# Kernel optimization log

Measured on AMD Instinct MI355X. Metric: run time of the kernel, lower is better.

Reference implementation:

```python
import jax, jax.numpy as jnp
import numpy as np

D_MODEL = 128
N_HEADS = 4
HEAD_DIM = D_MODEL // N_HEADS


def setup_inputs() -> dict:
    key = jax.random.key(0)
    ks = jax.random.split(key, 16)
    s = 0.05
    B, N, T = 1, 1024, 1024
    return {
        "node_states": jax.random.normal(ks[0], (B, N, D_MODEL), jnp.float32),
        "task_features": jax.random.normal(ks[1], (T, D_MODEL), jnp.float32),
        "in_proj_w": jax.random.normal(ks[2], (3 * D_MODEL, D_MODEL), jnp.float32) * s,
        "in_proj_b": jnp.zeros((3 * D_MODEL,), jnp.float32),
        "out_w": jax.random.normal(ks[3], (D_MODEL, D_MODEL), jnp.float32) * s,
        "out_b": jnp.zeros((D_MODEL,), jnp.float32),
        "W1": jax.random.normal(ks[4], (256, 256), jnp.float32) * s,
        "b1": jnp.zeros((256,), jnp.float32),
        "W2": jax.random.normal(ks[5], (128, 256), jnp.float32) * s,
        "b2": jnp.zeros((128,), jnp.float32),
        "W3": jax.random.normal(ks[6], (1, 128), jnp.float32) * s,
        "b3": jnp.zeros((1,), jnp.float32),
        "Wc1": jax.random.normal(ks[7], (256, D_MODEL), jnp.float32) * s,
        "bc1": jnp.zeros((256,), jnp.float32),
        "Wc2": jax.random.normal(ks[8], (32, 256), jnp.float32) * s,
        "bc2": jnp.zeros((32,), jnp.float32),
    }


def _mha(x, in_proj_w, in_proj_b, out_w, out_b):
    # x: [B, N, D]; torch nn.MultiheadAttention self-attention, batch_first.
    B, N, D = x.shape
    q = x @ in_proj_w[:D].T + in_proj_b[:D]
    k = x @ in_proj_w[D:2 * D].T + in_proj_b[D:2 * D]
    v = x @ in_proj_w[2 * D:].T + in_proj_b[2 * D:]
    def split(t):  # [B,N,D] -> [B,H,N,dh]
        return t.reshape(B, N, N_HEADS, HEAD_DIM).transpose(0, 2, 1, 3)
    qh, kh, vh = split(q), split(k), split(v)
    scores = jnp.einsum("bhqd,bhkd->bhqk", qh, kh) / jnp.sqrt(jnp.float32(HEAD_DIM))
    attn = jax.nn.softmax(scores, axis=-1)  # [B,H,N,N]
    ctx = jnp.einsum("bhqk,bhkd->bhqd", attn, vh)
    ctx = ctx.transpose(0, 2, 1, 3).reshape(B, N, D)
    out = ctx @ out_w.T + out_b
    attn_avg = attn.mean(axis=1)  # torch averages heads by default -> [B,N,N]
    return out, attn_avg


def reference(node_states, task_features, in_proj_w, in_proj_b, out_w, out_b,
              W1, b1, W2, b2, W3, b3, Wc1, bc1, Wc2, bc2):
    attended, attn_w = _mha(node_states, in_proj_w, in_proj_b, out_w, out_b)
    nodes = attended[0]  # original loop only uses batch 0: [N, D]
    # Linear on concat([task, node]) == split-weight sum; vectorize pairwise.
    t1 = task_features @ W1[:, :D_MODEL].T          # [T, 256]
    n1 = nodes @ W1[:, D_MODEL:].T                  # [N, 256]
    h1 = jax.nn.relu(t1[:, None, :] + n1[None, :, :] + b1)      # [T, N, 256]
    h2 = jax.nn.relu(jnp.einsum("tnc,kc->tnk", h1, W2) + b2)   # [T, N, 128]
    matching_scores = jax.nn.sigmoid(jnp.einsum("tnk,ok->tn", h2, W3) + b3[0])
    global_state = attended.mean(axis=1)            # [B, D]
    coordination_logits = jax.nn.relu(global_state @ Wc1.T + bc1) @ Wc2.T + bc2
    return matching_scores, coordination_logits, attn_w
```

## Files before the change

### kernel.cpp

```cpp
#include <hip/hip_runtime.h>
#include <hip/hip_fp16.h>
#include <stdint.h>


typedef __attribute__((ext_vector_type(4))) float floatx4;
typedef __attribute__((ext_vector_type(8))) _Float16 half8;

#define OFF_QKV  0x000000u
#define OFF_Q16  0x180000u
#define OFF_K16  0x1C0000u
#define OFF_V16  0x200000u
#define OFF_T1H  0x280000u
#define OFF_N1H  0x300000u
#define OFF_W2F  0x380000u
#define OFF_GS   0x398000u
#define OFF_SC   0x400000u
#define OFF_CTP  0xC00000u

__device__ __forceinline__ unsigned pkadd(unsigned a, unsigned b) {
    unsigned r; asm("v_pk_add_f16 %0, %1, %2" : "=v"(r) : "v"(a), "v"(b)); return r;
}
__device__ __forceinline__ unsigned pkmax(unsigned a, unsigned b) {
    unsigned r; asm("v_pk_max_f16 %0, %1, %2" : "=v"(r) : "v"(a), "v"(b)); return r;
}
__device__ __forceinline__ unsigned pk2h(float a, float b) {
    return (unsigned)__half_as_ushort(__float2half(a)) |
           ((unsigned)__half_as_ushort(__float2half(b)) << 16);
}
__device__ __forceinline__ float h2f(unsigned short u) {
    return __half2float(__ushort_as_half(u));
}
__device__ __forceinline__ unsigned short f2h(float v) {
    return __half_as_ushort(__float2half(v));
}

template<bool BIAS, bool F16OUT, bool SIDE>
__device__ __forceinline__ void gemm_dev(
    const float* __restrict__ A, int lda,
    const float* __restrict__ B, int ldb,
    const float* __restrict__ bias,
    void* __restrict__ Cv, int ldc, int K, float scale,
    int m0, int n0, float (*As)[64], float (*Bs)[64],
    unsigned short* __restrict__ q16o,
    unsigned short* __restrict__ k16o,
    unsigned short* __restrict__ v16o)
{
    const int tid = threadIdx.x;
    const int tx = tid & 15, ty = tid >> 4;
    const int lr = tid >> 2;
    const int lk = (tid & 3) * 4;
    float c[4][4] = {};

    for (int k0 = 0; k0 < K; k0 += 16) {
        float4 a  = *(const float4*)&A[(long)(m0 + lr) * lda + k0 + lk];
        float4 bb = *(const float4*)&B[(long)(n0 + lr) * ldb + k0 + lk];
        __syncthreads();
        As[lk + 0][lr] = a.x;  As[lk + 1][lr] = a.y;  As[lk + 2][lr] = a.z;  As[lk + 3][lr] = a.w;
        Bs[lk + 0][lr] = bb.x; Bs[lk + 1][lr] = bb.y; Bs[lk + 2][lr] = bb.z; Bs[lk + 3][lr] = bb.w;
        __syncthreads();
#pragma unroll
        for (int k = 0; k < 16; k++) {
            float4 av = *(const float4*)&As[k][ty * 4];
            float4 bv = *(const float4*)&Bs[k][tx * 4];
            c[0][0] += av.x * bv.x; c[0][1] += av.x * bv.y; c[0][2] += av.x * bv.z; c[0][3] += av.x * bv.w;
            c[1][0] += av.y * bv.x; c[1][1] += av.y * bv.y; c[1][2] += av.y * bv.z; c[1][3] += av.y * bv.w;
            c[2][0] += av.z * bv.x; c[2][1] += av.z * bv.y; c[2][2] += av.z * bv.z; c[2][3] += av.z * bv.w;
            c[3][0] += av.w * bv.x; c[3][1] += av.w * bv.y; c[3][2] += av.w * bv.z; c[3][3] += av.w * bv.w;
        }
    }

    float bsv[4] = {0.f, 0.f, 0.f, 0.f};
    if (BIAS) {
        float4 t = *(const float4*)&bias[n0 + tx * 4];
        bsv[0] = t.x; bsv[1] = t.y; bsv[2] = t.z; bsv[3] = t.w;
    }
    const int gcol = n0 + tx * 4;
#pragma unroll
    for (int i = 0; i < 4; i++) {
        float v0 = c[i][0] * scale + bsv[0];
        float v1 = c[i][1] * scale + bsv[1];
        float v2 = c[i][2] * scale + bsv[2];
        float v3 = c[i][3] * scale + bsv[3];
        long m = m0 + ty * 4 + i;
        if (F16OUT) {
            unsigned short* Cp = (unsigned short*)Cv;
            ushort4 o;
            o.x = f2h(v0); o.y = f2h(v1); o.z = f2h(v2); o.w = f2h(v3);
            *(ushort4*)&Cp[m * ldc + n0 + tx * 4] = o;
        } else {
            float* Cp = (float*)Cv;
            *(float4*)&Cp[m * ldc + n0 + tx * 4] = make_float4(v0, v1, v2, v3);
        }
        if (SIDE) {
            ushort4 o;
            o.x = f2h(v0); o.y = f2h(v1); o.z = f2h(v2); o.w = f2h(v3);
            if (gcol < 128) {
                *(ushort4*)&q16o[m * 128 + gcol] = o;
            } else if (gcol < 256) {
                *(ushort4*)&k16o[m * 128 + (gcol - 128)] = o;
            } else {
                v16o[(size_t)(gcol - 256 + 0) * 1024 + m] = o.x;
                v16o[(size_t)(gcol - 256 + 1) * 1024 + m] = o.y;
                v16o[(size_t)(gcol - 256 + 2) * 1024 + m] = o.z;
                v16o[(size_t)(gcol - 256 + 3) * 1024 + m] = o.w;
            }
        }
    }
}

__launch_bounds__(256)
__global__ void proj_fused(const float* __restrict__ node, const float* __restrict__ ipw,
                           const float* __restrict__ ipb,
                           const float* __restrict__ task, const float* __restrict__ W1,
                           const float* __restrict__ b1, const float* __restrict__ W2,
                           float* __restrict__ qkv, unsigned short* __restrict__ t1h,
                           unsigned short* __restrict__ w2f, float* __restrict__ gs,
                           unsigned short* __restrict__ q16,
                           unsigned short* __restrict__ k16,
                           unsigned short* __restrict__ v16t)
{
    __shared__ float As[16][64], Bs[16][64];
    const int bid = blockIdx.x;
    if (bid < 96) {
        gemm_dev<true, false, true>(node, 128, ipw, 128, ipb, qkv, 384, 128, 1.0f,
                                    (bid & 15) * 64, (bid >> 4) * 64, As, Bs,
                                    q16, k16, v16t);
    } else if (bid < 160) {
        const int b = bid - 96;
        gemm_dev<true, true, false>(task, 128, W1, 256, b1, t1h, 256, 128, 1.0f,
                                    (b & 15) * 64, (b >> 4) * 64, As, Bs,
                                    nullptr, nullptr, nullptr);
    } else if (bid < 176) {
        const int gtid = (bid - 160) * 256 + threadIdx.x;
        const int lane = gtid & 63, frag = gtid >> 6;
        const int cc = frag >> 3, ot = frag & 7;
        const float* src = &W2[(ot * 16 + (lane & 15)) * 256 + cc * 32 + (lane >> 4) * 8];
        uint4 o;
        o.x = pk2h(src[0], src[1]);
        o.y = pk2h(src[2], src[3]);
        o.z = pk2h(src[4], src[5]);
        o.w = pk2h(src[6], src[7]);
        ((uint4*)w2f)[gtid] = o;
    } else {
        if (threadIdx.x < 128) gs[threadIdx.x] = 0.f;
    }
}

__launch_bounds__(256)
__global__ void scores_mfma(const unsigned short* __restrict__ q16,
                            const unsigned short* __restrict__ k16,
                            unsigned short* __restrict__ sc16)
{
    const int h = blockIdx.z;
    const int tid = threadIdx.x;
    const int lane = tid & 63, wv = tid >> 6;
    const int col = lane & 15, quad = lane >> 4;
    const int q0 = blockIdx.x * 64 + wv * 16;
    const int kb = blockIdx.y * 64;
    unsigned short* dst = sc16 + ((size_t)h << 20);

    union { uint4 u; half8 h8; } bf;
    bf.u = *(const uint4*)&q16[(size_t)(q0 + col) * 128 + h * 32 + quad * 8];
#pragma unroll
    for (int kt = 0; kt < 4; kt++) {
        union { uint4 u; half8 h8; } af;
        af.u = *(const uint4*)&k16[(size_t)(kb + kt * 16 + col) * 128 + h * 32 + quad * 8];
        floatx4 c = {0.f, 0.f, 0.f, 0.f};
        c = __builtin_amdgcn_mfma_f32_16x16x32_f16(af.h8, bf.h8, c, 0, 0, 0);
        ushort4 o;
        o.x = f2h(c[0] * 0.17677669529663687f);
        o.y = f2h(c[1] * 0.17677669529663687f);
        o.z = f2h(c[2] * 0.17677669529663687f);
        o.w = f2h(c[3] * 0.17677669529663687f);
        *(ushort4*)&dst[(size_t)(q0 + col) * 1024 + kb + kt * 16 + quad * 4] = o;
    }
}

__launch_bounds__(256)
__global__ void attn_pre(const unsigned short* __restrict__ sc16,
                         unsigned short* __restrict__ pb,
                         float* __restrict__ attn_out)
{
    __shared__ float Ps[4][1024];
    __shared__ float stm[4], stl[4];
    const int t = threadIdx.x;
    const int q = blockIdx.x;

#pragma unroll
    for (int h = 0; h < 4; h++) {
        ushort4 u = *(const ushort4*)&sc16[((size_t)h << 20) + (size_t)q * 1024 + t * 4];
        *(float4*)&Ps[h][t * 4] = make_float4(h2f(u.x), h2f(u.y), h2f(u.z), h2f(u.w));
    }
    __syncthreads();

    {
        const int h = t >> 6, ln = t & 63;
        float4 v[4];
        float mx = -1e30f;
#pragma unroll
        for (int i = 0; i < 4; i++) {
            v[i] = *(const float4*)&Ps[h][ln * 4 + i * 256];
            mx = fmaxf(mx, fmaxf(fmaxf(v[i].x, v[i].y), fmaxf(v[i].z, v[i].w)));
        }
#pragma unroll
        for (int m = 1; m < 64; m <<= 1) mx = fmaxf(mx, __shfl_xor(mx, m));
        float s = 0.f;
#pragma unroll
        for (int i = 0; i < 4; i++)
            s += __expf(v[i].x - mx) + __expf(v[i].y - mx) +
                 __expf(v[i].z - mx) + __expf(v[i].w - mx);
#pragma unroll
        for (int m = 1; m < 64; m <<= 1) s += __shfl_xor(s, m);
        if (ln == 0) { stm[h] = mx; stl[h] = s; }
    }
    __syncthreads();

    float a0 = 0.f, a1 = 0.f, a2 = 0.f, a3 = 0.f;
#pragma unroll
    for (int h = 0; h < 4; h++) {
        const float m = stm[h], il = 1.0f / stl[h];
        float4 f = *(const float4*)&Ps[h][t * 4];
        float p0 = __expf(f.x - m) * il;
        float p1 = __expf(f.y - m) * il;
        float p2 = __expf(f.z - m) * il;
        float p3 = __expf(f.w - m) * il;
        a0 += p0; a1 += p1; a2 += p2; a3 += p3;
        ushort4 pw;
        pw.x = f2h(p0); pw.y = f2h(p1); pw.z = f2h(p2); pw.w = f2h(p3);
        *(ushort4*)&pb[((size_t)h << 20) + (size_t)q * 1024 + t * 4] = pw;
    }
    *(float4*)&attn_out[(size_t)q * 1024 + t * 4] =
        make_float4(0.25f * a0, 0.25f * a1, 0.25f * a2, 0.25f * a3);
}

__launch_bounds__(256)
__global__ void ctx_mfma(const unsigned short* __restrict__ pb,
                         const unsigned short* __restrict__ v16t,
                         float* __restrict__ ctxp)
{
    const int h = blockIdx.z;
    const int ks = blockIdx.y;
    const int q0 = blockIdx.x * 64;
    const int tid = threadIdx.x;
    const int lane = tid & 63, wv = tid >> 6;
    const int col = lane & 15, quad = lane >> 4;
    const unsigned short* ph = pb + ((size_t)h << 20);

    floatx4 acc[2] = {};
#pragma unroll
    for (int kst = 0; kst < 4; kst++) {
        const int k0 = ks * 128 + kst * 32;
        union { uint4 u; half8 h8; } pf;
        pf.u = *(const uint4*)&ph[(size_t)(q0 + wv * 16 + col) * 1024 + k0 + quad * 8];
#pragma unroll
        for (int dt = 0; dt < 2; dt++) {
            union { uint4 u; half8 h8; } vf;
            vf.u = *(const uint4*)&v16t[(size_t)(h * 32 + dt * 16 + col) * 1024 + k0 + quad * 8];
            acc[dt] = __builtin_amdgcn_mfma_f32_16x16x32_f16(vf.h8, pf.h8, acc[dt], 0, 0, 0);
        }
    }
#pragma unroll
    for (int dt = 0; dt < 2; dt++) {
        *(float4*)&ctxp[((size_t)ks * 1024 + q0 + wv * 16 + col) * 128 + h * 32 + dt * 16 + quad * 4] =
            make_float4(acc[dt][0], acc[dt][1], acc[dt][2], acc[dt][3]);
    }
}

__launch_bounds__(256)
__global__ void attn_post(const float* __restrict__ ctxp, const float* __restrict__ outw,
                          const float* __restrict__ outb, const float* __restrict__ W1,
                          unsigned short* __restrict__ n1h, float* __restrict__ gs)
{
    __shared__ float ctxs[4][128];
    __shared__ float attr[4][128];
    const int t = threadIdx.x;
    const int q0 = blockIdx.x * 4;

#pragma unroll
    for (int s = 0; s < 2; s++) {
        const int idx = s * 256 + t;
        const int q = idx >> 7, d = idx & 127;
        float v = 0.f;
#pragma unroll
        for (int ks = 0; ks < 8; ks++)
            v += ctxp[((size_t)ks * 1024 + (q0 + q)) * 128 + d];
        ctxs[q][d] = v;
    }
    __syncthreads();

    {
        const int j = t & 127, qp = t >> 7;
        float a0 = outb[j], a1 = a0;
        const float* wr = &outw[j * 128];
        for (int d = 0; d < 128; d += 4) {
            float4 w  = *(const float4*)&wr[d];
            float4 c0 = *(const float4*)&ctxs[qp * 2 + 0][d];
            float4 c1 = *(const float4*)&ctxs[qp * 2 + 1][d];
            a0 += w.x * c0.x + w.y * c0.y + w.z * c0.z + w.w * c0.w;
            a1 += w.x * c1.x + w.y * c1.y + w.z * c1.z + w.w * c1.w;
        }
        attr[qp * 2 + 0][j] = a0;
        attr[qp * 2 + 1][j] = a1;
    }
    __syncthreads();
    if (t < 128) atomicAdd(&gs[t], attr[0][t] + attr[1][t] + attr[2][t] + attr[3][t]);

    {
        const int c = t;
        const float* wr = &W1[c * 256 + 128];
        float n[4] = {};
        for (int d = 0; d < 128; d += 4) {
            float4 w = *(const float4*)&wr[d];
#pragma unroll
            for (int q = 0; q < 4; q++) {
                float4 a = *(const float4*)&attr[q][d];
                n[q] += w.x * a.x + w.y * a.y + w.z * a.z + w.w * a.w;
            }
        }
#pragma unroll
        for (int q = 0; q < 4; q++)
            n1h[(size_t)(q0 + q) * 256 + c] = __half_as_ushort(__float2half(n[q]));
    }
}

__launch_bounds__(256, 2)
__global__ void score_kernel(const unsigned short* __restrict__ t1h,
                             const unsigned short* __restrict__ n1h,
                             const unsigned short* __restrict__ w2f,
                             const float* __restrict__ b2, const float* __restrict__ W3,
                             const float* __restrict__ b3, float* __restrict__ out,
                             const float* __restrict__ gs,
                             const float* __restrict__ Wc1, const float* __restrict__ bc1,
                             const float* __restrict__ Wc2, const float* __restrict__ bc2,
                             float* __restrict__ outc)
{
    __shared__ unsigned short w2s[32768];
    __shared__ float b2s[128], w3s[128];
    const int tid = threadIdx.x;

    if (blockIdx.y == 32) {
        if (blockIdx.x != 0) return;
        float* g  = (float*)w2s;
        float* hh = g + 128;
        if (tid < 128) g[tid] = gs[tid] * (1.0f / 1024.0f);
        __syncthreads();
        {
            float a = bc1[tid];
            const float* wr = &Wc1[tid * 128];
            for (int d = 0; d < 128; d += 4) {
                float4 w = *(const float4*)&wr[d];
                a += w.x * g[d] + w.y * g[d + 1] + w.z * g[d + 2] + w.w * g[d + 3];
            }
            hh[tid] = fmaxf(a, 0.f);
        }
        __syncthreads();
        if (tid < 32) {
            float a = bc2[tid];
            const float* wr = &Wc2[tid * 256];
            for (int c = 0; c < 256; c += 4) {
                float4 w = *(const float4*)&wr[c];
                a += w.x * hh[c] + w.y * hh[c + 1] + w.z * hh[c + 2] + w.w * hh[c + 3];
            }
            outc[tid] = a;
        }
        return;
    }

    const int lane = tid & 63;
    const int wv = tid >> 6;
    const int col = lane & 15;
    const int quad = lane >> 4;
    const int nb = blockIdx.x * 64 + wv * 16;
    const int tb = blockIdx.y * 32;

    {
        const uint4* src = (const uint4*)w2f;
        uint4* dst = (uint4*)w2s;
#pragma unroll
        for (int i = 0; i < 16; i++) dst[tid + i * 256] = src[tid + i * 256];
        if (tid < 128) { b2s[tid] = b2[tid]; w3s[tid] = W3[tid]; }
    }

    const unsigned short* nbase = n1h + (size_t)(nb + col) * 256 + quad * 8;
    const unsigned short* tbase = t1h + (size_t)tb * 256 + quad * 8;
    const float b3s = b3[0];
    __syncthreads();

    uint4 np_c = *(const uint4*)(nbase);
    uint4 tp_c[4];
#pragma unroll
    for (int tt = 0; tt < 4; tt++)
        tp_c[tt] = *(const uint4*)(tbase + (size_t)tt * 256);

    for (int tg = 0; tg < 8; tg++) {
        floatx4 acc[4][8];
#pragma unroll
        for (int ot = 0; ot < 8; ot++) {
            float4 bq = *(const float4*)&b2s[ot * 16 + quad * 4];
            floatx4 bi = {bq.x, bq.y, bq.z, bq.w};
#pragma unroll
            for (int tt = 0; tt < 4; tt++) acc[tt][ot] = bi;
        }

#pragma unroll
        for (int cc = 0; cc < 8; cc++) {
            const int ncc = (cc + 1) & 7;
            const int ntg = (cc == 7) ? ((tg + 1) & 7) : tg;
            uint4 np_n = *(const uint4*)(nbase + ncc * 32);
            uint4 tp_n[4];
#pragma unroll
            for (int tt = 0; tt < 4; tt++)
                tp_n[tt] = *(const uint4*)(tbase + (size_t)(ntg * 4 + tt) * 256 + ncc * 32);

            const unsigned* npu = (const unsigned*)&np_c;
            union { unsigned u[4]; half8 h; } af[4];
#pragma unroll
            for (int tt = 0; tt < 4; tt++) {
                const unsigned* tpu = (const unsigned*)&tp_c[tt];
#pragma unroll
                for (int p = 0; p < 4; p++)
                    af[tt].u[p] = pkmax(pkadd(tpu[p], npu[p]), 0u);
            }
            __builtin_amdgcn_s_setprio(1);
#pragma unroll
            for (int ot = 0; ot < 8; ot++) {
                union { uint4 u; half8 h; } bf;
                bf.u = *(const uint4*)&w2s[((cc * 8 + ot) * 64 + lane) * 8];
#pragma unroll
                for (int tt = 0; tt < 4; tt++)
                    acc[tt][ot] = __builtin_amdgcn_mfma_f32_16x16x32_f16(bf.h, af[tt].h, acc[tt][ot], 0, 0, 0);
            }
            __builtin_amdgcn_s_setprio(0);

            np_c = np_n;
#pragma unroll
            for (int tt = 0; tt < 4; tt++) tp_c[tt] = tp_n[tt];
        }

        float part[4] = {0.f, 0.f, 0.f, 0.f};
#pragma unroll
        for (int ot = 0; ot < 8; ot++) {
            float4 wq = *(const float4*)&w3s[ot * 16 + quad * 4];
#pragma unroll
            for (int tt = 0; tt < 4; tt++) {
                floatx4 a = acc[tt][ot];
                part[tt] += fmaxf(a[0], 0.f) * wq.x + fmaxf(a[1], 0.f) * wq.y
                          + fmaxf(a[2], 0.f) * wq.z + fmaxf(a[3], 0.f) * wq.w;
            }
        }
        float outv = 0.f;
#pragma unroll
        for (int tt = 0; tt < 4; tt++) {
            float p = part[tt];
            p += __shfl_xor(p, 16);
            p += __shfl_xor(p, 32);
            if (quad == tt) outv = p;
        }
        out[(size_t)(tb + tg * 4 + quad) * 1024 + nb + col] =
            1.0f / (1.0f + __expf(-(outv + b3s)));
    }
}

extern "C" void kernel_launch(void* const* d_in, const int* in_sizes, int n_in,
                              void* d_out, int out_size, void* d_ws, size_t ws_size,
                              hipStream_t stream)
{
    const float* node = (const float*)d_in[0];
    const float* task = (const float*)d_in[1];
    const float* ipw  = (const float*)d_in[2];
    const float* ipb  = (const float*)d_in[3];
    const float* outw = (const float*)d_in[4];
    const float* outb = (const float*)d_in[5];
    const float* W1   = (const float*)d_in[6];
    const float* b1   = (const float*)d_in[7];
    const float* W2   = (const float*)d_in[8];
    const float* b2   = (const float*)d_in[9];
    const float* W3   = (const float*)d_in[10];
    const float* b3   = (const float*)d_in[11];
    const float* Wc1  = (const float*)d_in[12];
    const float* bc1  = (const float*)d_in[13];
    const float* Wc2  = (const float*)d_in[14];
    const float* bc2  = (const float*)d_in[15];

    char* ws = (char*)d_ws;
    float* qkv = (float*)(ws + OFF_QKV);
    unsigned short* q16 = (unsigned short*)(ws + OFF_Q16);
    unsigned short* k16 = (unsigned short*)(ws + OFF_K16);
    unsigned short* v16t = (unsigned short*)(ws + OFF_V16);
    unsigned short* t1h = (unsigned short*)(ws + OFF_T1H);
    unsigned short* n1h = (unsigned short*)(ws + OFF_N1H);
    unsigned short* w2f = (unsigned short*)(ws + OFF_W2F);
    float* gs = (float*)(ws + OFF_GS);
    unsigned short* sc16 = (unsigned short*)(ws + OFF_SC);
    float* ctxp = (float*)(ws + OFF_CTP);

    float* out_match = (float*)d_out;
    float* out_coord = out_match + 1048576;
    float* out_attn  = out_coord + 32;

    proj_fused<<<dim3(177, 1, 1), 256, 0, stream>>>(
        node, ipw, ipb, task, W1, b1, W2, qkv, t1h, w2f, gs, q16, k16, v16t);
    scores_mfma<<<dim3(16, 16, 4), 256, 0, stream>>>(q16, k16, sc16);
    attn_pre<<<dim3(1024, 1, 1), 256, 0, stream>>>(sc16, sc16, out_attn);
    ctx_mfma<<<dim3(16, 8, 4), 256, 0, stream>>>(sc16, v16t, ctxp);
    attn_post<<<dim3(256, 1, 1), 256, 0, stream>>>(ctxp, outw, outb, W1, n1h, gs);
    score_kernel<<<dim3(16, 33, 1), 256, 0, stream>>>(
        t1h, n1h, w2f, b2, W3, b3, out_match,
        gs, Wc1, bc1, Wc2, bc2, out_coord);
}
```

Before: 193.9 us.

## Fuse attention scores, softmax, context and output projection into one kernel

Replaces four kernels (scores, softmax, context, post-projection) with a single kernel that keeps each 16-query block's full fp16 score rows for all heads in swizzled LDS, then does softmax, P·V, head averaging, out-projection and the W1 node projection in place. This removes the global round trips of the 8 MB score buffer and the context partial sums, plus three launches. In exchange it launches only 64 blocks of 512 threads with about 144 KB of dynamic shared memory each, which leaves many CUs idle and exposes K and V load latency.

```diff
diff --git a/kernel.cpp b/kernel.cpp
--- a/kernel.cpp
+++ b/kernel.cpp
@@ -14,8 +14,6 @@
 #define OFF_N1H  0x300000u
 #define OFF_W2F  0x380000u
 #define OFF_GS   0x398000u
-#define OFF_SC   0x400000u
-#define OFF_CTP  0xC00000u
 
 __device__ __forceinline__ unsigned pkadd(unsigned a, unsigned b) {
     unsigned r; asm("v_pk_add_f16 %0, %1, %2" : "=v"(r) : "v"(a), "v"(b)); return r;
@@ -32,6 +30,9 @@
 }
 __device__ __forceinline__ unsigned short f2h(float v) {
     return __half_as_ushort(__float2half(v));
+}
+__device__ __forceinline__ int plds(int row, int kb) {
+    return row * 2048 + (((kb & ~15) ^ ((row & 7) << 4))) + (kb & 15);
 }
 
 template<bool BIAS, bool F16OUT, bool SIDE>
@@ -146,180 +147,174 @@
     }
 }
 
-__launch_bounds__(256)
-__global__ void scores_mfma(const unsigned short* __restrict__ q16,
-                            const unsigned short* __restrict__ k16,
-                            unsigned short* __restrict__ sc16)
+__launch_bounds__(512)
+__global__ void attn_one(const unsigned short* __restrict__ q16,
+                         const unsigned short* __restrict__ k16,
+                         const unsigned short* __restrict__ v16t,
+                         const float* __restrict__ outw, const float* __restrict__ outb,
+                         const float* __restrict__ W1,
+                         unsigned short* __restrict__ n1h, float* __restrict__ gs,
+                         float* __restrict__ attn_out)
 {
-    const int h = blockIdx.z;
+    extern __shared__ char smem[];
+    float* ctx2 = (float*)(smem + 131072);
+    float* il   = (float*)(smem + 147456);
+    float* attr = (float*)smem;
+
     const int tid = threadIdx.x;
+    const int q0 = blockIdx.x * 16;
     const int lane = tid & 63, wv = tid >> 6;
     const int col = lane & 15, quad = lane >> 4;
-    const int q0 = blockIdx.x * 64 + wv * 16;
-    const int kb = blockIdx.y * 64;
-    unsigned short* dst = sc16 + ((size_t)h << 20);
-
-    union { uint4 u; half8 h8; } bf;
-    bf.u = *(const uint4*)&q16[(size_t)(q0 + col) * 128 + h * 32 + quad * 8];
-#pragma unroll
-    for (int kt = 0; kt < 4; kt++) {
-        union { uint4 u; half8 h8; } af;
-        af.u = *(const uint4*)&k16[(size_t)(kb + kt * 16 + col) * 128 + h * 32 + quad * 8];
-        floatx4 c = {0.f, 0.f, 0.f, 0.f};
-        c = __builtin_amdgcn_mfma_f32_16x16x32_f16(af.h8, bf.h8, c, 0, 0, 0);
-        ushort4 o;
-        o.x = f2h(c[0] * 0.17677669529663687f);
-        o.y = f2h(c[1] * 0.17677669529663687f);
-        o.z = f2h(c[2] * 0.17677669529663687f);
-        o.w = f2h(c[3] * 0.17677669529663687f);
-        *(ushort4*)&dst[(size_t)(q0 + col) * 1024 + kb + kt * 16 + quad * 4] = o;
-    }
-}
-
-__launch_bounds__(256)
-__global__ void attn_pre(const unsigned short* __restrict__ sc16,
-                         unsigned short* __restrict__ pb,
-                         float* __restrict__ attn_out)
-{
-    __shared__ float Ps[4][1024];
-    __shared__ float stm[4], stl[4];
-    const int t = threadIdx.x;
-    const int q = blockIdx.x;
-
-#pragma unroll
-    for (int h = 0; h < 4; h++) {
-        ushort4 u = *(const ushort4*)&sc16[((size_t)h << 20) + (size_t)q * 1024 + t * 4];
-        *(float4*)&Ps[h][t * 4] = make_float4(h2f(u.x), h2f(u.y), h2f(u.z), h2f(u.w));
+    const int h = wv & 3, khalf = wv >> 2;
+    const int prow = h * 16 + col;
+
+    {
+        union { uint4 u; half8 h8; } bq;
+        bq.u = *(const uint4*)&q16[(size_t)(q0 + col) * 128 + h * 32 + quad * 8];
+        for (int kt = khalf * 32; kt < khalf * 32 + 32; kt++) {
+            union { uint4 u; half8 h8; } ak;
+            ak.u = *(const uint4*)&k16[(size_t)(kt * 16 + col) * 128 + h * 32 + quad * 8];
+            floatx4 c = {0.f, 0.f, 0.f, 0.f};
+            c = __builtin_amdgcn_mfma_f32_16x16x32_f16(ak.h8, bq.h8, c, 0, 0, 0);
+            ushort4 o;
+            o.x = f2h(c[0] * 0.17677669529663687f);
+            o.y = f2h(c[1] * 0.17677669529663687f);
+            o.z = f2h(c[2] * 0.17677669529663687f);
+            o.w = f2h(c[3] * 0.17677669529663687f);
+            *(ushort4*)(smem + plds(prow, kt * 32 + quad * 8)) = o;
+        }
     }
     __syncthreads();
 
     {
-        const int h = t >> 6, ln = t & 63;
-        float4 v[4];
+        const int row = tid >> 3, oct = tid & 7;
+        char* rb = smem + row * 2048;
+        const int swz = (row & 7) << 4;
         float mx = -1e30f;
 #pragma unroll
-        for (int i = 0; i < 4; i++) {
-            v[i] = *(const float4*)&Ps[h][ln * 4 + i * 256];
-            mx = fmaxf(mx, fmaxf(fmaxf(v[i].x, v[i].y), fmaxf(v[i].z, v[i].w)));
-        }
-#pragma unroll
-        for (int m = 1; m < 64; m <<= 1) mx = fmaxf(mx, __shfl_xor(mx, m));
+        for (int i = 0; i < 16; i++) {
+            uint4 v = *(uint4*)(rb + ((oct * 256 + i * 16) ^ swz));
+            const unsigned short* pv = (const unsigned short*)&v;
+#pragma unroll
+            for (int j = 0; j < 8; j++) mx = fmaxf(mx, h2f(pv[j]));
+        }
+        mx = fmaxf(mx, __shfl_xor(mx, 1));
+        mx = fmaxf(mx, __shfl_xor(mx, 2));
+        mx = fmaxf(mx, __shfl_xor(mx, 4));
         float s = 0.f;
 #pragma unroll
-        for (int i = 0; i < 4; i++)
-            s += __expf(v[i].x - mx) + __expf(v[i].y - mx) +
-                 __expf(v[i].z - mx) + __expf(v[i].w - mx);
-#pragma unroll
-        for (int m = 1; m < 64; m <<= 1) s += __shfl_xor(s, m);
-        if (ln == 0) { stm[h] = mx; stl[h] = s; }
+        for (int i = 0; i < 16; i++) {
+            char* ap = rb + ((oct * 256 + i * 16) ^ swz);
+            uint4 v = *(uint4*)ap;
+            const unsigned short* pv = (const unsigned short*)&v;
+            ushort4 w0, w1;
+            float p0 = __expf(h2f(pv[0]) - mx), p1 = __expf(h2f(pv[1]) - mx);
+            float p2 = __expf(h2f(pv[2]) - mx), p3 = __expf(h2f(pv[3]) - mx);
+            float p4 = __expf(h2f(pv[4]) - mx), p5 = __expf(h2f(pv[5]) - mx);
+            float p6 = __expf(h2f(pv[6]) - mx), p7 = __expf(h2f(pv[7]) - mx);
+            s += p0 + p1 + p2 + p3 + p4 + p5 + p6 + p7;
+            w0.x = f2h(p0); w0.y = f2h(p1); w0.z = f2h(p2); w0.w = f2h(p3);
+            w1.x = f2h(p4); w1.y = f2h(p5); w1.z = f2h(p6); w1.w = f2h(p7);
+            *(ushort4*)ap = w0;
+            *(ushort4*)(ap + 8) = w1;
+        }
+        s += __shfl_xor(s, 1);
+        s += __shfl_xor(s, 2);
+        s += __shfl_xor(s, 4);
+        if ((tid & 7) == 0) il[row] = 1.0f / s;
     }
     __syncthreads();
 
-    float a0 = 0.f, a1 = 0.f, a2 = 0.f, a3 = 0.f;
-#pragma unroll
-    for (int h = 0; h < 4; h++) {
-        const float m = stm[h], il = 1.0f / stl[h];
-        float4 f = *(const float4*)&Ps[h][t * 4];
-        float p0 = __expf(f.x - m) * il;
-        float p1 = __expf(f.y - m) * il;
-        float p2 = __expf(f.z - m) * il;
-        float p3 = __expf(f.w - m) * il;
-        a0 += p0; a1 += p1; a2 += p2; a3 += p3;
-        ushort4 pw;
-        pw.x = f2h(p0); pw.y = f2h(p1); pw.z = f2h(p2); pw.w = f2h(p3);
-        *(ushort4*)&pb[((size_t)h << 20) + (size_t)q * 1024 + t * 4] = pw;
-    }
-    *(float4*)&attn_out[(size_t)q * 1024 + t * 4] =
-        make_float4(0.25f * a0, 0.25f * a1, 0.25f * a2, 0.25f * a3);
-}
-
-__launch_bounds__(256)
-__global__ void ctx_mfma(const unsigned short* __restrict__ pb,
-                         const unsigned short* __restrict__ v16t,
-                         float* __restrict__ ctxp)
-{
-    const int h = blockIdx.z;
-    const int ks = blockIdx.y;
-    const int q0 = blockIdx.x * 64;
-    const int tid = threadIdx.x;
-    const int lane = tid & 63, wv = tid >> 6;
-    const int col = lane & 15, quad = lane >> 4;
-    const unsigned short* ph = pb + ((size_t)h << 20);
-
-    floatx4 acc[2] = {};
-#pragma unroll
-    for (int kst = 0; kst < 4; kst++) {
-        const int k0 = ks * 128 + kst * 32;
-        union { uint4 u; half8 h8; } pf;
-        pf.u = *(const uint4*)&ph[(size_t)(q0 + wv * 16 + col) * 1024 + k0 + quad * 8];
+    {
+        floatx4 acc[2] = {};
+        for (int ks = khalf * 16; ks < khalf * 16 + 16; ks++) {
+            union { uint4 u; half8 h8; } pf;
+            pf.u = *(uint4*)(smem + plds(prow, ks * 64 + quad * 16));
+#pragma unroll
+            for (int dt = 0; dt < 2; dt++) {
+                union { uint4 u; half8 h8; } vf;
+                vf.u = *(const uint4*)&v16t[(size_t)(h * 32 + dt * 16 + col) * 1024 + ks * 32 + quad * 8];
+                acc[dt] = __builtin_amdgcn_mfma_f32_16x16x32_f16(vf.h8, pf.h8, acc[dt], 0, 0, 0);
+            }
+        }
+        const float sil = il[prow];
 #pragma unroll
         for (int dt = 0; dt < 2; dt++) {
-            union { uint4 u; half8 h8; } vf;
-            vf.u = *(const uint4*)&v16t[(size_t)(h * 32 + dt * 16 + col) * 1024 + k0 + quad * 8];
-            acc[dt] = __builtin_amdgcn_mfma_f32_16x16x32_f16(vf.h8, pf.h8, acc[dt], 0, 0, 0);
-        }
-    }
-#pragma unroll
-    for (int dt = 0; dt < 2; dt++) {
-        *(float4*)&ctxp[((size_t)ks * 1024 + q0 + wv * 16 + col) * 128 + h * 32 + dt * 16 + quad * 4] =
-            make_float4(acc[dt][0], acc[dt][1], acc[dt][2], acc[dt][3]);
-    }
-}
-
-__launch_bounds__(256)
-__global__ void attn_post(const float* __restrict__ ctxp, const float* __restrict__ outw,
-                          const float* __restrict__ outb, const float* __restrict__ W1,
-                          unsigned short* __restrict__ n1h, float* __restrict__ gs)
-{
-    __shared__ float ctxs[4][128];
-    __shared__ float attr[4][128];
-    const int t = threadIdx.x;
-    const int q0 = blockIdx.x * 4;
-
-#pragma unroll
-    for (int s = 0; s < 2; s++) {
-        const int idx = s * 256 + t;
-        const int q = idx >> 7, d = idx & 127;
-        float v = 0.f;
-#pragma unroll
-        for (int ks = 0; ks < 8; ks++)
-            v += ctxp[((size_t)ks * 1024 + (q0 + q)) * 128 + d];
-        ctxs[q][d] = v;
+            *(float4*)&ctx2[(khalf * 16 + col) * 128 + h * 32 + dt * 16 + quad * 4] =
+                make_float4(acc[dt][0] * sil, acc[dt][1] * sil, acc[dt][2] * sil, acc[dt][3] * sil);
+        }
+    }
+    {
+        const int q = tid >> 5, kc = tid & 31;
+        const float s0 = il[q] * 0.25f, s1 = il[16 + q] * 0.25f;
+        const float s2 = il[32 + q] * 0.25f, s3 = il[48 + q] * 0.25f;
+#pragma unroll
+        for (int b = 0; b < 4; b++) {
+            const int kb = kc * 64 + b * 16;
+            uint4 v0 = *(uint4*)(smem + plds(q, kb));
+            uint4 v1 = *(uint4*)(smem + plds(16 + q, kb));
+            uint4 v2 = *(uint4*)(smem + plds(32 + q, kb));
+            uint4 v3 = *(uint4*)(smem + plds(48 + q, kb));
+            const unsigned short* p0 = (const unsigned short*)&v0;
+            const unsigned short* p1 = (const unsigned short*)&v1;
+            const unsigned short* p2 = (const unsigned short*)&v2;
+            const unsigned short* p3 = (const unsigned short*)&v3;
+            float o[8];
+#pragma unroll
+            for (int j = 0; j < 8; j++)
+                o[j] = h2f(p0[j]) * s0 + h2f(p1[j]) * s1 + h2f(p2[j]) * s2 + h2f(p3[j]) * s3;
+            float* dst = &attn_out[(size_t)(q0 + q) * 1024 + kc * 32 + b * 8];
+            *(float4*)dst = make_float4(o[0], o[1], o[2], o[3]);
+            *(float4*)(dst + 4) = make_float4(o[4], o[5], o[6], o[7]);
+        }
     }
     __syncthreads();
 
     {
-        const int j = t & 127, qp = t >> 7;
-        float a0 = outb[j], a1 = a0;
+        const int j = tid & 127, qh = tid >> 7;
+        float a0 = outb[j], a1 = a0, a2 = a0, a3 = a0;
         const float* wr = &outw[j * 128];
         for (int d = 0; d < 128; d += 4) {
-            float4 w  = *(const float4*)&wr[d];
-            float4 c0 = *(const float4*)&ctxs[qp * 2 + 0][d];
-            float4 c1 = *(const float4*)&ctxs[qp * 2 + 1][d];
-            a0 += w.x * c0.x + w.y * c0.y + w.z * c0.z + w.w * c0.w;
-            a1 += w.x * c1.x + w.y * c1.y + w.z * c1.z + w.w * c1.w;
-        }
-        attr[qp * 2 + 0][j] = a0;
-        attr[qp * 2 + 1][j] = a1;
+            float4 w = *(const float4*)&wr[d];
+#pragma unroll
+            for (int qq = 0; qq < 4; qq++) {
+                const int q = qh * 4 + qq;
+                float4 c0 = *(const float4*)&ctx2[q * 128 + d];
+                float4 c1 = *(const float4*)&ctx2[(16 + q) * 128 + d];
+                float dot = w.x * (c0.x + c1.x) + w.y * (c0.y + c1.y)
+                          + w.z * (c0.z + c1.z) + w.w * (c0.w + c1.w);
+                if (qq == 0) a0 += dot; else if (qq == 1) a1 += dot;
+                else if (qq == 2) a2 += dot; else a3 += dot;
+            }
+        }
+        attr[(qh * 4 + 0) * 128 + j] = a0;
+        attr[(qh * 4 + 1) * 128 + j] = a1;
+        attr[(qh * 4 + 2) * 128 + j] = a2;
+        attr[(qh * 4 + 3) * 128 + j] = a3;
     }
     __syncthreads();
-    if (t < 128) atomicAdd(&gs[t], attr[0][t] + attr[1][t] + attr[2][t] + attr[3][t]);
-
-    {
-        const int c = t;
+
+    if (tid < 128) {
+        float s = 0.f;
+#pragma unroll
+        for (int q = 0; q < 16; q++) s += attr[q * 128 + tid];
+        atomicAdd(&gs[tid], s);
+    }
+    {
+        const int c = tid & 255, qh = tid >> 8;
         const float* wr = &W1[c * 256 + 128];
-        float n[4] = {};
+        float n[8] = {};
         for (int d = 0; d < 128; d += 4) {
             float4 w = *(const float4*)&wr[d];
 #pragma unroll
-            for (int q = 0; q < 4; q++) {
-                float4 a = *(const float4*)&attr[q][d];
-                n[q] += w.x * a.x + w.y * a.y + w.z * a.z + w.w * a.w;
-            }
-        }
-#pragma unroll
-        for (int q = 0; q < 4; q++)
-            n1h[(size_t)(q0 + q) * 256 + c] = __half_as_ushort(__float2half(n[q]));
+            for (int qq = 0; qq < 8; qq++) {
+                float4 a = *(const float4*)&attr[(qh * 8 + qq) * 128 + d];
+                n[qq] += w.x * a.x + w.y * a.y + w.z * a.z + w.w * a.w;
+            }
+        }
+#pragma unroll
+        for (int qq = 0; qq < 8; qq++)
+            n1h[(size_t)(q0 + qh * 8 + qq) * 256 + c] = f2h(n[qq]);
     }
 }
 
@@ -491,19 +486,22 @@
     unsigned short* n1h = (unsigned short*)(ws + OFF_N1H);
     unsigned short* w2f = (unsigned short*)(ws + OFF_W2F);
     float* gs = (float*)(ws + OFF_GS);
-    unsigned short* sc16 = (unsigned short*)(ws + OFF_SC);
-    float* ctxp = (float*)(ws + OFF_CTP);
 
     float* out_match = (float*)d_out;
     float* out_coord = out_match + 1048576;
     float* out_attn  = out_coord + 32;
 
+    static bool attr_set = false;
+    if (!attr_set) {
+        hipFuncSetAttribute((const void*)attn_one,
+                            hipFuncAttributeMaxDynamicSharedMemorySize, 147712);
+        attr_set = true;
+    }
+
     proj_fused<<<dim3(177, 1, 1), 256, 0, stream>>>(
         node, ipw, ipb, task, W1, b1, W2, qkv, t1h, w2f, gs, q16, k16, v16t);
-    scores_mfma<<<dim3(16, 16, 4), 256, 0, stream>>>(q16, k16, sc16);
-    attn_pre<<<dim3(1024, 1, 1), 256, 0, stream>>>(sc16, sc16, out_attn);
-    ctx_mfma<<<dim3(16, 8, 4), 256, 0, stream>>>(sc16, v16t, ctxp);
-    attn_post<<<dim3(256, 1, 1), 256, 0, stream>>>(ctxp, outw, outb, W1, n1h, gs);
+    attn_one<<<dim3(64, 1, 1), 512, 147712, stream>>>(
+        q16, k16, v16t, outw, outb, W1, n1h, gs, out_attn);
     score_kernel<<<dim3(16, 33, 1), 256, 0, stream>>>(
         t1h, n1h, w2f, b2, W3, b3, out_match,
         gs, Wc1, bc1, Wc2, bc2, out_coord);
```

Result: slower. 203.8 us (+5.1%).
